# Performance work log

Measured on AMD Instinct MI355X. Metric: run time of the kernel, lower is better.

Reference implementation:

```python
import jax, jax.numpy as jnp
import numpy as np

B, S, H = 32, 2048, 1024
UNITS = 1024


def setup_inputs() -> dict:
    key = jax.random.key(0)
    ks = jax.random.split(key, 8)
    scale_h = 1.0 / np.sqrt(H)
    scale_u = 1.0 / np.sqrt(UNITS)
    return {
        "query": jax.random.normal(ks[0], (B, H), dtype=jnp.float32),
        "values": jax.random.normal(ks[1], (B, S, H), dtype=jnp.float32),
        "W1": jax.random.normal(ks[2], (H, UNITS), dtype=jnp.float32) * scale_h,
        "b1": jnp.zeros((UNITS,), dtype=jnp.float32),
        "W2": jax.random.normal(ks[3], (H, UNITS), dtype=jnp.float32) * scale_h,
        "b2": jnp.zeros((UNITS,), dtype=jnp.float32),
        "V": jax.random.normal(ks[4], (UNITS, 1), dtype=jnp.float32) * scale_u,
        "bv": jnp.zeros((1,), dtype=jnp.float32),
    }


def reference(query, values, W1, b1, W2, b2, V, bv):
    # proj_v: [B, S, units]; proj_q: [B, 1, units] (query expanded on time axis)
    proj_v = jnp.einsum("bsh,hu->bsu", values, W1) + b1
    proj_q = (query @ W2 + b2)[:, None, :]
    # score: [B, S, 1]
    score = jnp.tanh(proj_v + proj_q) @ V + bv
    attention_weights = jax.nn.softmax(score, axis=1)  # softmax over seq axis
    context_vector = jnp.sum(attention_weights * values, axis=1)  # [B, H]
    return context_vector, attention_weights
```

## Files before the change

### kernel.cpp

```cpp
#include <hip/hip_runtime.h>

#define H 1024
#define UNITS 1024
#define BATCH 32
#define SEQ 2048
#define M_TOT (BATCH * SEQ)

typedef __attribute__((ext_vector_type(8))) short bf16x8;
typedef __attribute__((ext_vector_type(8))) unsigned short u16x8;
typedef __attribute__((ext_vector_type(4))) float f32x4;

__device__ __forceinline__ unsigned short f2bf(float f) {
  union { float f; unsigned u; } x; x.f = f;
  unsigned r = x.u + 0x7FFFu + ((x.u >> 16) & 1u);
  return (unsigned short)(r >> 16);
}
__device__ __forceinline__ float bf2f(unsigned short h) {
  union { unsigned u; float f; } x; x.u = (unsigned)h << 16;
  return x.f;
}

__device__ __forceinline__ void gll16(const unsigned short* g, unsigned short* l) {
  __builtin_amdgcn_global_load_lds(
      (const __attribute__((address_space(1))) void*)g,
      (__attribute__((address_space(3))) void*)l, 16, 0, 0);
}

__global__ void k_cast(const float* __restrict__ in, unsigned short* __restrict__ out) {
  size_t i = ((size_t)blockIdx.x * 256 + threadIdx.x) * 8;
  float4 v0 = *reinterpret_cast<const float4*>(in + i);
  float4 v1 = *reinterpret_cast<const float4*>(in + i + 4);
  union { unsigned short h[8]; u16x8 v; } p;
  p.h[0] = f2bf(v0.x); p.h[1] = f2bf(v0.y); p.h[2] = f2bf(v0.z); p.h[3] = f2bf(v0.w);
  p.h[4] = f2bf(v1.x); p.h[5] = f2bf(v1.y); p.h[6] = f2bf(v1.z); p.h[7] = f2bf(v1.w);
  *reinterpret_cast<u16x8*>(out + i) = p.v;
}

__global__ void k_transpose_w1(const float* __restrict__ W1, unsigned short* __restrict__ W1T) {
  __shared__ float tile[32][33];
  int bx = blockIdx.x, by = blockIdx.y;
  int tx = threadIdx.x, ty = threadIdx.y;
#pragma unroll
  for (int i = 0; i < 4; ++i)
    tile[ty + i * 8][tx] = W1[(by * 32 + ty + i * 8) * UNITS + bx * 32 + tx];
  __syncthreads();
#pragma unroll
  for (int i = 0; i < 4; ++i)
    W1T[(bx * 32 + ty + i * 8) * H + by * 32 + tx] = f2bf(tile[tx][ty + i * 8]);
}

__global__ void k_projq(const float* __restrict__ query, const float* __restrict__ W2,
                        const float* __restrict__ b2, float* __restrict__ projq) {
  __shared__ float q[H];
  int b = blockIdx.x;
  int u = blockIdx.y * 256 + threadIdx.x;
  for (int i = threadIdx.x; i < H; i += 256) q[i] = query[b * H + i];
  __syncthreads();
  float acc = 0.f;
#pragma unroll 8
  for (int k = 0; k < H; ++k) acc = fmaf(q[k], W2[k * UNITS + u], acc);
  projq[b * UNITS + u] = acc + b2[u];
}

#define BM 256
#define BN 256
#define NT 16

__global__ __launch_bounds__(512, 2) void k_score3(
    const unsigned short* __restrict__ Vb,
    const unsigned short* __restrict__ W1T,
    const float* __restrict__ b1,
    const float* __restrict__ projq,
    const float* __restrict__ V,
    float* __restrict__ scores)
{
  __shared__ unsigned short As[2][2][256][32];
  __shared__ unsigned short Bs[2][2][256][32];

  const int tid = threadIdx.x;
  const int lane = tid & 63;
  const int wave = tid >> 6;
  const int wm = wave >> 2;
  const int wn = wave & 3;
  const int li = lane & 15, hi = lane >> 4;
  const int csw = ((hi ^ (li >> 2)) & 3) << 3;

  const int g = blockIdx.x;
  const int xcd = g & 7;
  const int local = g >> 3;
  const int n_t = local & 3;
  const int m_t = xcd + ((local >> 2) << 3);
  const int m0 = m_t * BM;
  const int n0 = n_t * BN;

  const int srow = wave * 32 + (lane >> 2);
  const int scol = (((lane & 3) ^ ((lane >> 4) & 3)) << 3);

  auto STAGE_A = [&](int bf, int kt, int kh) {
    const unsigned short* src =
        Vb + (size_t)(m0 + srow) * H + kt * 64 + kh * 32 + scol;
    unsigned short* dst = &As[bf][kh][wave * 32][0];
    gll16(src, dst);
    gll16(src + (size_t)16 * H, dst + 16 * 32);
  };
  auto STAGE_B = [&](int bf, int kt, int kh) {
    const unsigned short* src =
        W1T + (size_t)(n0 + srow) * H + kt * 64 + kh * 32 + scol;
    unsigned short* dst = &Bs[bf][kh][wave * 32][0];
    gll16(src, dst);
    gll16(src + (size_t)16 * H, dst + 16 * 32);
  };

  f32x4 acc[8][4] = {};

  STAGE_A(0, 0, 0);
  STAGE_B(0, 0, 0);
  STAGE_A(0, 0, 1);
  STAGE_B(0, 0, 1);

#pragma unroll 2
  for (int c = 0; c < NT; ++c) {
    const int buf = c & 1, nbuf = buf ^ 1;
    const int cn = (c < NT - 1) ? c + 1 : NT - 1;

    bf16x8 a[8], b0, b1v;

    asm volatile("s_waitcnt vmcnt(4)" ::: "memory");
    __builtin_amdgcn_s_barrier();
    STAGE_A(nbuf, cn, 0);
#pragma unroll
    for (int i = 0; i < 8; ++i)
      a[i] = *reinterpret_cast<const bf16x8*>(&As[buf][0][wm * 128 + i * 16 + li][csw]);
    b0  = *reinterpret_cast<const bf16x8*>(&Bs[buf][0][wn * 64 + 0 * 16 + li][csw]);
    b1v = *reinterpret_cast<const bf16x8*>(&Bs[buf][0][wn * 64 + 1 * 16 + li][csw]);
    __builtin_amdgcn_s_setprio(1);
#pragma unroll
    for (int i = 0; i < 8; ++i) {
      acc[i][0] = __builtin_amdgcn_mfma_f32_16x16x32_bf16(a[i], b0, acc[i][0], 0, 0, 0);
      acc[i][1] = __builtin_amdgcn_mfma_f32_16x16x32_bf16(a[i], b1v, acc[i][1], 0, 0, 0);
    }
    __builtin_amdgcn_s_setprio(0);

    STAGE_B(nbuf, cn, 0);
    b0  = *reinterpret_cast<const bf16x8*>(&Bs[buf][0][wn * 64 + 2 * 16 + li][csw]);
    b1v = *reinterpret_cast<const bf16x8*>(&Bs[buf][0][wn * 64 + 3 * 16 + li][csw]);
    __builtin_amdgcn_s_setprio(1);
#pragma unroll
    for (int i = 0; i < 8; ++i) {
      acc[i][2] = __builtin_amdgcn_mfma_f32_16x16x32_bf16(a[i], b0, acc[i][2], 0, 0, 0);
      acc[i][3] = __builtin_amdgcn_mfma_f32_16x16x32_bf16(a[i], b1v, acc[i][3], 0, 0, 0);
    }
    __builtin_amdgcn_s_setprio(0);

    asm volatile("s_waitcnt vmcnt(4)" ::: "memory");
    __builtin_amdgcn_s_barrier();
    STAGE_A(nbuf, cn, 1);
#pragma unroll
    for (int i = 0; i < 8; ++i)
      a[i] = *reinterpret_cast<const bf16x8*>(&As[buf][1][wm * 128 + i * 16 + li][csw]);
    b0  = *reinterpret_cast<const bf16x8*>(&Bs[buf][1][wn * 64 + 0 * 16 + li][csw]);
    b1v = *reinterpret_cast<const bf16x8*>(&Bs[buf][1][wn * 64 + 1 * 16 + li][csw]);
    __builtin_amdgcn_s_setprio(1);
#pragma unroll
    for (int i = 0; i < 8; ++i) {
      acc[i][0] = __builtin_amdgcn_mfma_f32_16x16x32_bf16(a[i], b0, acc[i][0], 0, 0, 0);
      acc[i][1] = __builtin_amdgcn_mfma_f32_16x16x32_bf16(a[i], b1v, acc[i][1], 0, 0, 0);
    }
    __builtin_amdgcn_s_setprio(0);

    STAGE_B(nbuf, cn, 1);
    b0  = *reinterpret_cast<const bf16x8*>(&Bs[buf][1][wn * 64 + 2 * 16 + li][csw]);
    b1v = *reinterpret_cast<const bf16x8*>(&Bs[buf][1][wn * 64 + 3 * 16 + li][csw]);
    __builtin_amdgcn_s_setprio(1);
#pragma unroll
    for (int i = 0; i < 8; ++i) {
      acc[i][2] = __builtin_amdgcn_mfma_f32_16x16x32_bf16(a[i], b0, acc[i][2], 0, 0, 0);
      acc[i][3] = __builtin_amdgcn_mfma_f32_16x16x32_bf16(a[i], b1v, acc[i][3], 0, 0, 0);
    }
    __builtin_amdgcn_s_setprio(0);
  }

  const int b = m0 >> 11;
  float bias[4], vv[4];
#pragma unroll
  for (int j = 0; j < 4; ++j) {
    int u = n0 + wn * 64 + j * 16 + li;
    bias[j] = b1[u] + projq[b * UNITS + u];
    vv[j] = V[u];
  }
#pragma unroll
  for (int mi = 0; mi < 8; ++mi) {
#pragma unroll
    for (int r = 0; r < 4; ++r) {
      float s = 0.f;
#pragma unroll
      for (int j = 0; j < 4; ++j) {
        float x = acc[mi][j][r] + bias[j];
        float e = __expf(2.f * x);
        s += (1.f - 2.f / (e + 1.f)) * vv[j];
      }
      s += __shfl_xor(s, 1);
      s += __shfl_xor(s, 2);
      s += __shfl_xor(s, 4);
      s += __shfl_xor(s, 8);
      if (li == 0) {
        int row = m0 + wm * 128 + mi * 16 + hi * 4 + r;
        atomicAdd(&scores[row], s);
      }
    }
  }
}

#define FBM 128
#define FBN 128
#define FBK 64
#define LDK 72
__global__ __launch_bounds__(256) void k_score_f32(
    const float* __restrict__ values, const unsigned short* __restrict__ W1T,
    const float* __restrict__ b1, const float* __restrict__ projq,
    const float* __restrict__ V, float* __restrict__ scores)
{
  __shared__ unsigned short Asf[FBM][LDK];
  __shared__ unsigned short Bsf[FBN][LDK];
  const int tid = threadIdx.x;
  const int lane = tid & 63;
  const int wave = tid >> 6;
  const int wm = wave >> 1, wn = wave & 1;
  const int li = lane & 15, hi = lane >> 4;
  const int n0 = blockIdx.x * FBN;
  const int m0 = blockIdx.y * FBM;
  f32x4 acc[4][4] = {};
  for (int k0 = 0; k0 < H; k0 += FBK) {
    __syncthreads();
#pragma unroll
    for (int q = 0; q < 8; ++q) {
      int idx = q * 256 + tid;
      int row = idx >> 4;
      int kc = (idx & 15) << 2;
      float4 v = *reinterpret_cast<const float4*>(&values[(size_t)(m0 + row) * H + k0 + kc]);
      union { unsigned short h[4]; unsigned long long u64; } p;
      p.h[0] = f2bf(v.x); p.h[1] = f2bf(v.y); p.h[2] = f2bf(v.z); p.h[3] = f2bf(v.w);
      *reinterpret_cast<unsigned long long*>(&Asf[row][kc]) = p.u64;
    }
#pragma unroll
    for (int q = 0; q < 4; ++q) {
      int idx = q * 256 + tid;
      int row = idx >> 3;
      int kc = (idx & 7) << 3;
      *reinterpret_cast<u16x8*>(&Bsf[row][kc]) =
          *reinterpret_cast<const u16x8*>(&W1T[(size_t)(n0 + row) * H + k0 + kc]);
    }
    __syncthreads();
#pragma unroll
    for (int ks = 0; ks < 2; ++ks) {
      const int kofs = ks * 32 + 8 * hi;
      bf16x8 a[4], bb[4];
#pragma unroll
      for (int i = 0; i < 4; ++i)
        a[i] = *reinterpret_cast<const bf16x8*>(&Asf[wm * 64 + i * 16 + li][kofs]);
#pragma unroll
      for (int i = 0; i < 4; ++i)
        bb[i] = *reinterpret_cast<const bf16x8*>(&Bsf[wn * 64 + i * 16 + li][kofs]);
#pragma unroll
      for (int mi = 0; mi < 4; ++mi)
#pragma unroll
        for (int ni = 0; ni < 4; ++ni)
          acc[mi][ni] = __builtin_amdgcn_mfma_f32_16x16x32_bf16(a[mi], bb[ni], acc[mi][ni], 0, 0, 0);
    }
  }
  const int b = m0 >> 11;
  float bias[4], vv[4];
#pragma unroll
  for (int ni = 0; ni < 4; ++ni) {
    int u = n0 + wn * 64 + ni * 16 + li;
    bias[ni] = b1[u] + projq[b * UNITS + u];
    vv[ni] = V[u];
  }
#pragma unroll
  for (int mi = 0; mi < 4; ++mi) {
#pragma unroll
    for (int r = 0; r < 4; ++r) {
      float s = 0.f;
#pragma unroll
      for (int ni = 0; ni < 4; ++ni) {
        float x = acc[mi][ni][r] + bias[ni];
        float e = __expf(2.f * x);
        s += (1.f - 2.f / (e + 1.f)) * vv[ni];
      }
      s += __shfl_xor(s, 1);
      s += __shfl_xor(s, 2);
      s += __shfl_xor(s, 4);
      s += __shfl_xor(s, 8);
      if (li == 0) atomicAdd(&scores[m0 + wm * 64 + mi * 16 + hi * 4 + r], s);
    }
  }
}

__global__ void k_softmax(const float* __restrict__ scores, float* __restrict__ wts) {
  __shared__ float red[8];
  int b = blockIdx.x;
  int t = threadIdx.x;
  float v[8];
  float mx = -3.4e38f;
#pragma unroll
  for (int i = 0; i < 8; ++i) {
    v[i] = scores[b * SEQ + i * 256 + t];
    mx = fmaxf(mx, v[i]);
  }
#pragma unroll
  for (int o = 1; o < 64; o <<= 1) mx = fmaxf(mx, __shfl_xor(mx, o));
  if ((t & 63) == 0) red[t >> 6] = mx;
  __syncthreads();
  mx = fmaxf(fmaxf(red[0], red[1]), fmaxf(red[2], red[3]));
  float sum = 0.f;
#pragma unroll
  for (int i = 0; i < 8; ++i) { v[i] = __expf(v[i] - mx); sum += v[i]; }
#pragma unroll
  for (int o = 1; o < 64; o <<= 1) sum += __shfl_xor(sum, o);
  if ((t & 63) == 0) red[4 + (t >> 6)] = sum;
  __syncthreads();
  float inv = 1.f / (red[4] + red[5] + red[6] + red[7]);
#pragma unroll
  for (int i = 0; i < 8; ++i) wts[b * SEQ + i * 256 + t] = v[i] * inv;
}

__global__ void k_context_bf(const unsigned short* __restrict__ Vb,
                             const float* __restrict__ wts, float* __restrict__ ctx) {
  int b = blockIdx.x, sc = blockIdx.y;
  int h4 = threadIdx.x * 4;
  const unsigned short* vb = Vb + (size_t)b * SEQ * H;
  float a0 = 0, a1 = 0, a2 = 0, a3 = 0;
  int s0 = sc * 128;
#pragma unroll 4
  for (int s = s0; s < s0 + 128; ++s) {
    float w = wts[b * SEQ + s];
    ushort4 v = *reinterpret_cast<const ushort4*>(&vb[(size_t)s * H + h4]);
    a0 = fmaf(w, bf2f(v.x), a0);
    a1 = fmaf(w, bf2f(v.y), a1);
    a2 = fmaf(w, bf2f(v.z), a2);
    a3 = fmaf(w, bf2f(v.w), a3);
  }
  atomicAdd(&ctx[b * H + h4 + 0], a0);
  atomicAdd(&ctx[b * H + h4 + 1], a1);
  atomicAdd(&ctx[b * H + h4 + 2], a2);
  atomicAdd(&ctx[b * H + h4 + 3], a3);
}

__global__ void k_context(const float* __restrict__ values, const float* __restrict__ wts,
                          float* __restrict__ ctx) {
  int b = blockIdx.x, hc = blockIdx.y, sc = blockIdx.z;
  int h = hc * 256 + threadIdx.x;
  const float* vb = values + (size_t)b * SEQ * H;
  float acc = 0.f;
  int s0 = sc * 128;
#pragma unroll 4
  for (int s = s0; s < s0 + 128; ++s)
    acc = fmaf(wts[b * SEQ + s], vb[(size_t)s * H + h], acc);
  atomicAdd(&ctx[b * H + h], acc);
}

extern "C" void kernel_launch(void* const* d_in, const int* in_sizes, int n_in,
                              void* d_out, int out_size, void* d_ws, size_t ws_size,
                              hipStream_t stream) {
  (void)in_sizes; (void)n_in; (void)out_size;
  const float* query  = (const float*)d_in[0];
  const float* values = (const float*)d_in[1];
  const float* W1     = (const float*)d_in[2];
  const float* b1     = (const float*)d_in[3];
  const float* W2     = (const float*)d_in[4];
  const float* b2     = (const float*)d_in[5];
  const float* V      = (const float*)d_in[6];

  float* out = (float*)d_out;
  float* ctx = out;
  float* wts = out + BATCH * H;

  const size_t vb_bytes = (size_t)M_TOT * H * 2;
  const size_t need = vb_bytes + (2u << 20) + (256u << 10) + (128u << 10);

  if (ws_size >= need) {
    char* ws = (char*)d_ws;
    unsigned short* Vb  = (unsigned short*)ws;
    unsigned short* W1T = (unsigned short*)(ws + vb_bytes);
    float* scores = (float*)(ws + vb_bytes + (2u << 20));
    float* projq  = (float*)(ws + vb_bytes + (2u << 20) + (256u << 10));

    hipMemsetAsync(scores, 0, M_TOT * sizeof(float), stream);
    hipMemsetAsync(ctx, 0, BATCH * H * sizeof(float), stream);

    k_cast<<<(M_TOT * H / 8) / 256, 256, 0, stream>>>(values, Vb);
    k_transpose_w1<<<dim3(32, 32), dim3(32, 8), 0, stream>>>(W1, W1T);
    k_projq<<<dim3(32, 4), 256, 0, stream>>>(query, W2, b2, projq);
    k_score3<<<(M_TOT / BM) * (UNITS / BN), 512, 0, stream>>>(Vb, W1T, b1, projq, V, scores);
    k_softmax<<<BATCH, 256, 0, stream>>>(scores, wts);
    k_context_bf<<<dim3(BATCH, 16), 256, 0, stream>>>(Vb, wts, ctx);
  } else {
    char* ws = (char*)d_ws;
    unsigned short* W1T = (unsigned short*)ws;
    float* scores = (float*)(ws + (2u << 20));
    float* projq  = (float*)(ws + (2u << 20) + (256u << 10));

    hipMemsetAsync(scores, 0, M_TOT * sizeof(float), stream);
    hipMemsetAsync(ctx, 0, BATCH * H * sizeof(float), stream);

    k_transpose_w1<<<dim3(32, 32), dim3(32, 8), 0, stream>>>(W1, W1T);
    k_projq<<<dim3(32, 4), 256, 0, stream>>>(query, W2, b2, projq);
    k_score_f32<<<dim3(UNITS / FBN, M_TOT / FBM), 256, 0, stream>>>(values, W1T, b1, projq, V, scores);
    k_softmax<<<BATCH, 256, 0, stream>>>(scores, wts);
    k_context<<<dim3(BATCH, H / 256, 16), 256, 0, stream>>>(values, wts, ctx);
  }
}
```

Baseline: 343.9 us.

## Use unified 64-wide LDS tiles with XOR swizzle and one barrier per K-step

Restructures the shared-memory tiles of the score GEMM from two 32-column halves into a single 64-column row layout with an 8-way XOR swizzle. Each K-step is now staged as a whole, with one vmcnt(0) wait and one barrier instead of two partial waits and barriers. This is meant to cut barrier overhead and LDS bank conflicts. In exchange, the full wait drains all outstanding loads, so next-tile prefetch overlaps less with compute.

Result: no change. 341.1 us (-0.8%).

```diff
diff --git a/kernel.cpp b/kernel.cpp
--- a/kernel.cpp
+++ b/kernel.cpp
@@ -74,8 +74,8 @@
     const float* __restrict__ V,
     float* __restrict__ scores)
 {
-  __shared__ unsigned short As[2][2][256][32];
-  __shared__ unsigned short Bs[2][2][256][32];
+  __shared__ unsigned short As[2][256][64];
+  __shared__ unsigned short Bs[2][256][64];
 
   const int tid = threadIdx.x;
   const int lane = tid & 63;
@@ -83,7 +83,7 @@
   const int wm = wave >> 2;
   const int wn = wave & 3;
   const int li = lane & 15, hi = lane >> 4;
-  const int csw = ((hi ^ (li >> 2)) & 3) << 3;
+  const int lx = li & 7;
 
   const int g = blockIdx.x;
   const int xcd = g & 7;
@@ -93,46 +93,46 @@
   const int m0 = m_t * BM;
   const int n0 = n_t * BN;
 
-  const int srow = wave * 32 + (lane >> 2);
-  const int scol = (((lane & 3) ^ ((lane >> 4) & 3)) << 3);
-
-  auto STAGE_A = [&](int bf, int kt, int kh) {
-    const unsigned short* src =
-        Vb + (size_t)(m0 + srow) * H + kt * 64 + kh * 32 + scol;
-    unsigned short* dst = &As[bf][kh][wave * 32][0];
-    gll16(src, dst);
-    gll16(src + (size_t)16 * H, dst + 16 * 32);
+  const int crow = lane >> 3;
+  const int scol = ((lane & 7) ^ crow) << 3;
+
+  auto STAGE_A = [&](int bf, int kt) {
+#pragma unroll
+    for (int q = 0; q < 4; ++q) {
+      int r = wave * 32 + q * 8;
+      gll16(&Vb[(size_t)(m0 + r + crow) * H + kt * 64 + scol], &As[bf][r][0]);
+    }
   };
-  auto STAGE_B = [&](int bf, int kt, int kh) {
-    const unsigned short* src =
-        W1T + (size_t)(n0 + srow) * H + kt * 64 + kh * 32 + scol;
-    unsigned short* dst = &Bs[bf][kh][wave * 32][0];
-    gll16(src, dst);
-    gll16(src + (size_t)16 * H, dst + 16 * 32);
+  auto STAGE_B = [&](int bf, int kt) {
+#pragma unroll
+    for (int q = 0; q < 4; ++q) {
+      int r = wave * 32 + q * 8;
+      gll16(&W1T[(size_t)(n0 + r + crow) * H + kt * 64 + scol], &Bs[bf][r][0]);
+    }
   };
 
   f32x4 acc[8][4] = {};
 
-  STAGE_A(0, 0, 0);
-  STAGE_B(0, 0, 0);
-  STAGE_A(0, 0, 1);
-  STAGE_B(0, 0, 1);
+  STAGE_A(0, 0);
+  STAGE_B(0, 0);
 
 #pragma unroll 2
   for (int c = 0; c < NT; ++c) {
     const int buf = c & 1, nbuf = buf ^ 1;
     const int cn = (c < NT - 1) ? c + 1 : NT - 1;
 
+    asm volatile("s_waitcnt vmcnt(0)" ::: "memory");
+    __builtin_amdgcn_s_barrier();
+
     bf16x8 a[8], b0, b1v;
 
-    asm volatile("s_waitcnt vmcnt(4)" ::: "memory");
-    __builtin_amdgcn_s_barrier();
-    STAGE_A(nbuf, cn, 0);
+    STAGE_A(nbuf, cn);
 #pragma unroll
     for (int i = 0; i < 8; ++i)
-      a[i] = *reinterpret_cast<const bf16x8*>(&As[buf][0][wm * 128 + i * 16 + li][csw]);
-    b0  = *reinterpret_cast<const bf16x8*>(&Bs[buf][0][wn * 64 + 0 * 16 + li][csw]);
-    b1v = *reinterpret_cast<const bf16x8*>(&Bs[buf][0][wn * 64 + 1 * 16 + li][csw]);
+      a[i] = *reinterpret_cast<const bf16x8*>(
+          &As[buf][wm * 128 + i * 16 + li][(hi ^ lx) << 3]);
+    b0  = *reinterpret_cast<const bf16x8*>(&Bs[buf][wn * 64 +  0 + li][(hi ^ lx) << 3]);
+    b1v = *reinterpret_cast<const bf16x8*>(&Bs[buf][wn * 64 + 16 + li][(hi ^ lx) << 3]);
     __builtin_amdgcn_s_setprio(1);
 #pragma unroll
     for (int i = 0; i < 8; ++i) {
@@ -141,9 +141,9 @@
     }
     __builtin_amdgcn_s_setprio(0);
 
-    STAGE_B(nbuf, cn, 0);
-    b0  = *reinterpret_cast<const bf16x8*>(&Bs[buf][0][wn * 64 + 2 * 16 + li][csw]);
-    b1v = *reinterpret_cast<const bf16x8*>(&Bs[buf][0][wn * 64 + 3 * 16 + li][csw]);
+    STAGE_B(nbuf, cn);
+    b0  = *reinterpret_cast<const bf16x8*>(&Bs[buf][wn * 64 + 32 + li][(hi ^ lx) << 3]);
+    b1v = *reinterpret_cast<const bf16x8*>(&Bs[buf][wn * 64 + 48 + li][(hi ^ lx) << 3]);
     __builtin_amdgcn_s_setprio(1);
 #pragma unroll
     for (int i = 0; i < 8; ++i) {
@@ -152,14 +152,12 @@
     }
     __builtin_amdgcn_s_setprio(0);
 
-    asm volatile("s_waitcnt vmcnt(4)" ::: "memory");
-    __builtin_amdgcn_s_barrier();
-    STAGE_A(nbuf, cn, 1);
 #pragma unroll
     for (int i = 0; i < 8; ++i)
-      a[i] = *reinterpret_cast<const bf16x8*>(&As[buf][1][wm * 128 + i * 16 + li][csw]);
-    b0  = *reinterpret_cast<const bf16x8*>(&Bs[buf][1][wn * 64 + 0 * 16 + li][csw]);
-    b1v = *reinterpret_cast<const bf16x8*>(&Bs[buf][1][wn * 64 + 1 * 16 + li][csw]);
+      a[i] = *reinterpret_cast<const bf16x8*>(
+          &As[buf][wm * 128 + i * 16 + li][((4 + hi) ^ lx) << 3]);
+    b0  = *reinterpret_cast<const bf16x8*>(&Bs[buf][wn * 64 +  0 + li][((4 + hi) ^ lx) << 3]);
+    b1v = *reinterpret_cast<const bf16x8*>(&Bs[buf][wn * 64 + 16 + li][((4 + hi) ^ lx) << 3]);
     __builtin_amdgcn_s_setprio(1);
 #pragma unroll
     for (int i = 0; i < 8; ++i) {
@@ -168,9 +166,8 @@
     }
     __builtin_amdgcn_s_setprio(0);
 
-    STAGE_B(nbuf, cn, 1);
-    b0  = *reinterpret_cast<const bf16x8*>(&Bs[buf][1][wn * 64 + 2 * 16 + li][csw]);
-    b1v = *reinterpret_cast<const bf16x8*>(&Bs[buf][1][wn * 64 + 3 * 16 + li][csw]);
+    b0  = *reinterpret_cast<const bf16x8*>(&Bs[buf][wn * 64 + 32 + li][((4 + hi) ^ lx) << 3]);
+    b1v = *reinterpret_cast<const bf16x8*>(&Bs[buf][wn * 64 + 48 + li][((4 + hi) ^ lx) << 3]);
     __builtin_amdgcn_s_setprio(1);
 #pragma unroll
     for (int i = 0; i < 8; ++i) {
```

## Repack LDS tiles as paired rows with XOR swizzle and add explicit MFMA scheduling

Applied to the files above, without the earlier changes.

Changes the shared-memory layout of the A/B tiles from 256x32 to 128x64 with two logical rows packed per physical row and a new XOR swizzle for both staging and fragment reads, aiming to cut LDS bank conflicts. It also reorders each phase so fragment loads come before issuing the next global-to-LDS stage, waits on lgkmcnt with sched_barrier before the MFMA burst, and adds extra workgroup barriers after each MFMA group plus a final vmcnt(0) drain. The extra barriers add synchronisation cost in exchange for tighter overlap control.

After: 348.7 us. Within noise of the previous version (+1.4%).

```diff
diff --git a/kernel.cpp b/kernel.cpp
--- a/kernel.cpp
+++ b/kernel.cpp
@@ -64,7 +64,7 @@
 
 #define BM 256
 #define BN 256
-#define NT 16
+#define NKT 16
 
 __global__ __launch_bounds__(512, 2) void k_score3(
     const unsigned short* __restrict__ Vb,
@@ -74,8 +74,8 @@
     const float* __restrict__ V,
     float* __restrict__ scores)
 {
-  __shared__ unsigned short As[2][2][256][32];
-  __shared__ unsigned short Bs[2][2][256][32];
+  __shared__ unsigned short As[2][2][128][64];
+  __shared__ unsigned short Bs[2][2][128][64];
 
   const int tid = threadIdx.x;
   const int lane = tid & 63;
@@ -83,7 +83,8 @@
   const int wm = wave >> 2;
   const int wn = wave & 3;
   const int li = lane & 15, hi = lane >> 4;
-  const int csw = ((hi ^ (li >> 2)) & 3) << 3;
+  const int lr2 = li >> 1;
+  const int pcol = (((((li & 1) << 2) + hi) ^ lr2) & 7) << 3;
 
   const int g = blockIdx.x;
   const int xcd = g & 7;
@@ -93,25 +94,29 @@
   const int m0 = m_t * BM;
   const int n0 = n_t * BN;
 
-  const int srow = wave * 32 + (lane >> 2);
-  const int scol = (((lane & 3) ^ ((lane >> 4) & 3)) << 3);
+  const int sL = (lane & 7) ^ (lane >> 3);
+  const int srow = 2 * (lane >> 3) + (sL >> 2);
+  const int scol = (sL & 3) << 3;
 
   auto STAGE_A = [&](int bf, int kt, int kh) {
-    const unsigned short* src =
-        Vb + (size_t)(m0 + srow) * H + kt * 64 + kh * 32 + scol;
-    unsigned short* dst = &As[bf][kh][wave * 32][0];
-    gll16(src, dst);
-    gll16(src + (size_t)16 * H, dst + 16 * 32);
+#pragma unroll
+    for (int q = 0; q < 2; ++q) {
+      int mb = wave * 32 + q * 16;
+      gll16(&Vb[(size_t)(m0 + mb + srow) * H + kt * 64 + kh * 32 + scol],
+            &As[bf][kh][wave * 16 + q * 8][0]);
+    }
   };
   auto STAGE_B = [&](int bf, int kt, int kh) {
-    const unsigned short* src =
-        W1T + (size_t)(n0 + srow) * H + kt * 64 + kh * 32 + scol;
-    unsigned short* dst = &Bs[bf][kh][wave * 32][0];
-    gll16(src, dst);
-    gll16(src + (size_t)16 * H, dst + 16 * 32);
+#pragma unroll
+    for (int q = 0; q < 2; ++q) {
+      int mb = wave * 32 + q * 16;
+      gll16(&W1T[(size_t)(n0 + mb + srow) * H + kt * 64 + kh * 32 + scol],
+            &Bs[bf][kh][wave * 16 + q * 8][0]);
+    }
   };
 
   f32x4 acc[8][4] = {};
+  bf16x8 a[8], bL0, bL1, bH0, bH1;
 
   STAGE_A(0, 0, 0);
   STAGE_B(0, 0, 0);
@@ -119,66 +124,79 @@
   STAGE_B(0, 0, 1);
 
 #pragma unroll 2
-  for (int c = 0; c < NT; ++c) {
+  for (int c = 0; c < NKT; ++c) {
     const int buf = c & 1, nbuf = buf ^ 1;
-    const int cn = (c < NT - 1) ? c + 1 : NT - 1;
-
-    bf16x8 a[8], b0, b1v;
+    const int cn = (c + 1 < NKT) ? c + 1 : NKT - 1;
 
     asm volatile("s_waitcnt vmcnt(4)" ::: "memory");
     __builtin_amdgcn_s_barrier();
+#pragma unroll
+    for (int i = 0; i < 8; ++i)
+      a[i] = *reinterpret_cast<const bf16x8*>(&As[buf][0][wm * 64 + i * 8 + lr2][pcol]);
+    bL0 = *reinterpret_cast<const bf16x8*>(&Bs[buf][0][wn * 32 + 0 * 8 + lr2][pcol]);
+    bL1 = *reinterpret_cast<const bf16x8*>(&Bs[buf][0][wn * 32 + 1 * 8 + lr2][pcol]);
     STAGE_A(nbuf, cn, 0);
+    asm volatile("s_waitcnt lgkmcnt(0)" ::: "memory");
+    __builtin_amdgcn_sched_barrier(0);
+    __builtin_amdgcn_s_setprio(1);
+#pragma unroll
+    for (int i = 0; i < 8; ++i) {
+      acc[i][0] = __builtin_amdgcn_mfma_f32_16x16x32_bf16(a[i], bL0, acc[i][0], 0, 0, 0);
+      acc[i][1] = __builtin_amdgcn_mfma_f32_16x16x32_bf16(a[i], bL1, acc[i][1], 0, 0, 0);
+    }
+    __builtin_amdgcn_s_setprio(0);
+    __builtin_amdgcn_s_barrier();
+
+    bH0 = *reinterpret_cast<const bf16x8*>(&Bs[buf][0][wn * 32 + 2 * 8 + lr2][pcol]);
+    bH1 = *reinterpret_cast<const bf16x8*>(&Bs[buf][0][wn * 32 + 3 * 8 + lr2][pcol]);
+    STAGE_B(nbuf, cn, 0);
+    asm volatile("s_waitcnt lgkmcnt(0)" ::: "memory");
+    __builtin_amdgcn_sched_barrier(0);
+    __builtin_amdgcn_s_setprio(1);
+#pragma unroll
+    for (int i = 0; i < 8; ++i) {
+      acc[i][2] = __builtin_amdgcn_mfma_f32_16x16x32_bf16(a[i], bH0, acc[i][2], 0, 0, 0);
+      acc[i][3] = __builtin_amdgcn_mfma_f32_16x16x32_bf16(a[i], bH1, acc[i][3], 0, 0, 0);
+    }
+    __builtin_amdgcn_s_setprio(0);
+    __builtin_amdgcn_s_barrier();
+
+    asm volatile("s_waitcnt vmcnt(4)" ::: "memory");
+    __builtin_amdgcn_s_barrier();
 #pragma unroll
     for (int i = 0; i < 8; ++i)
-      a[i] = *reinterpret_cast<const bf16x8*>(&As[buf][0][wm * 128 + i * 16 + li][csw]);
-    b0  = *reinterpret_cast<const bf16x8*>(&Bs[buf][0][wn * 64 + 0 * 16 + li][csw]);
-    b1v = *reinterpret_cast<const bf16x8*>(&Bs[buf][0][wn * 64 + 1 * 16 + li][csw]);
+      a[i] = *reinterpret_cast<const bf16x8*>(&As[buf][1][wm * 64 + i * 8 + lr2][pcol]);
+    bL0 = *reinterpret_cast<const bf16x8*>(&Bs[buf][1][wn * 32 + 0 * 8 + lr2][pcol]);
+    bL1 = *reinterpret_cast<const bf16x8*>(&Bs[buf][1][wn * 32 + 1 * 8 + lr2][pcol]);
+    STAGE_A(nbuf, cn, 1);
+    asm volatile("s_waitcnt lgkmcnt(0)" ::: "memory");
+    __builtin_amdgcn_sched_barrier(0);
     __builtin_amdgcn_s_setprio(1);
 #pragma unroll
     for (int i = 0; i < 8; ++i) {
-      acc[i][0] = __builtin_amdgcn_mfma_f32_16x16x32_bf16(a[i], b0, acc[i][0], 0, 0, 0);
-      acc[i][1] = __builtin_amdgcn_mfma_f32_16x16x32_bf16(a[i], b1v, acc[i][1], 0, 0, 0);
+      acc[i][0] = __builtin_amdgcn_mfma_f32_16x16x32_bf16(a[i], bL0, acc[i][0], 0, 0, 0);
+      acc[i][1] = __builtin_amdgcn_mfma_f32_16x16x32_bf16(a[i], bL1, acc[i][1], 0, 0, 0);
     }
     __builtin_amdgcn_s_setprio(0);
-
-    STAGE_B(nbuf, cn, 0);
-    b0  = *reinterpret_cast<const bf16x8*>(&Bs[buf][0][wn * 64 + 2 * 16 + li][csw]);
-    b1v = *reinterpret_cast<const bf16x8*>(&Bs[buf][0][wn * 64 + 3 * 16 + li][csw]);
+    __builtin_amdgcn_s_barrier();
+
+    bH0 = *reinterpret_cast<const bf16x8*>(&Bs[buf][1][wn * 32 + 2 * 8 + lr2][pcol]);
+    bH1 = *reinterpret_cast<const bf16x8*>(&Bs[buf][1][wn * 32 + 3 * 8 + lr2][pcol]);
+    STAGE_B(nbuf, cn, 1);
+    asm volatile("s_waitcnt lgkmcnt(0)" ::: "memory");
+    __builtin_amdgcn_sched_barrier(0);
     __builtin_amdgcn_s_setprio(1);
 #pragma unroll
     for (int i = 0; i < 8; ++i) {
-      acc[i][2] = __builtin_amdgcn_mfma_f32_16x16x32_bf16(a[i], b0, acc[i][2], 0, 0, 0);
-      acc[i][3] = __builtin_amdgcn_mfma_f32_16x16x32_bf16(a[i], b1v, acc[i][3], 0, 0, 0);
+      acc[i][2] = __builtin_amdgcn_mfma_f32_16x16x32_bf16(a[i], bH0, acc[i][2], 0, 0, 0);
+      acc[i][3] = __builtin_amdgcn_mfma_f32_16x16x32_bf16(a[i], bH1, acc[i][3], 0, 0, 0);
     }
     __builtin_amdgcn_s_setprio(0);
-
-    asm volatile("s_waitcnt vmcnt(4)" ::: "memory");
-    __builtin_amdgcn_s_barrier();
-    STAGE_A(nbuf, cn, 1);
-#pragma unroll
-    for (int i = 0; i < 8; ++i)
-      a[i] = *reinterpret_cast<const bf16x8*>(&As[buf][1][wm * 128 + i * 16 + li][csw]);
-    b0  = *reinterpret_cast<const bf16x8*>(&Bs[buf][1][wn * 64 + 0 * 16 + li][csw]);
-    b1v = *reinterpret_cast<const bf16x8*>(&Bs[buf][1][wn * 64 + 1 * 16 + li][csw]);
-    __builtin_amdgcn_s_setprio(1);
-#pragma unroll
-    for (int i = 0; i < 8; ++i) {
-      acc[i][0] = __builtin_amdgcn_mfma_f32_16x16x32_bf16(a[i], b0, acc[i][0], 0, 0, 0);
-      acc[i][1] = __builtin_amdgcn_mfma_f32_16x16x32_bf16(a[i], b1v, acc[i][1], 0, 0, 0);
-    }
-    __builtin_amdgcn_s_setprio(0);
-
-    STAGE_B(nbuf, cn, 1);
-    b0  = *reinterpret_cast<const bf16x8*>(&Bs[buf][1][wn * 64 + 2 * 16 + li][csw]);
-    b1v = *reinterpret_cast<const bf16x8*>(&Bs[buf][1][wn * 64 + 3 * 16 + li][csw]);
-    __builtin_amdgcn_s_setprio(1);
-#pragma unroll
-    for (int i = 0; i < 8; ++i) {
-      acc[i][2] = __builtin_amdgcn_mfma_f32_16x16x32_bf16(a[i], b0, acc[i][2], 0, 0, 0);
-      acc[i][3] = __builtin_amdgcn_mfma_f32_16x16x32_bf16(a[i], b1v, acc[i][3], 0, 0, 0);
-    }
-    __builtin_amdgcn_s_setprio(0);
-  }
+    __builtin_amdgcn_s_barrier();
+  }
+
+  asm volatile("s_waitcnt vmcnt(0)" ::: "memory");
+  __builtin_amdgcn_s_barrier();
 
   const int b = m0 >> 11;
   float bias[4], vv[4];
```
